# Kernel optimization log

Hardware: AMD Instinct MI355X
Metric: run time of the kernel (lower is better)

## Reference

```python
import jax, jax.numpy as jnp
import numpy as np

CHUNKS = 4  # number of input-feature chunks (seg_mode='input')
QMAX = 127.0  # symmetric int8 fake-quant range
EPS = 1e-8


def setup_inputs() -> dict:
    key = jax.random.key(0)
    k1, k2, k3 = jax.random.split(key, 3)
    B, S, F, O = 4, 4096, 4096, 4096
    x = jax.random.normal(k1, (B, S, F), dtype=jnp.float32)
    weight = jax.random.normal(k2, (O, F), dtype=jnp.float32) * 0.02
    bias = jax.random.normal(k3, (O,), dtype=jnp.float32) * 0.02
    return {"x": x, "weight": weight, "bias": bias}


def _fake_quant(t, scale):
    # symmetric int8 fake quantization: quantize then dequantize in float
    return jnp.clip(jnp.round(t / scale), -QMAX, QMAX) * scale


def reference(x, weight, bias):
    B, S, F = x.shape
    O = weight.shape[0]
    C = CHUNKS
    d = F // C

    # single weight quantizer (seg_mode='input'): per-tensor fake quant of full weight
    w_scale = jnp.maximum(jnp.max(jnp.abs(weight)) / QMAX, EPS)
    w_fq = _fake_quant(weight, w_scale)          # [O, F]
    wc = w_fq.reshape(O, C, d)                   # chunked along in_features

    # per-chunk input quantizers: one per input chunk
    xc = x.reshape(B, S, C, d)                   # split input along last dim
    x_scale = jnp.maximum(
        jnp.max(jnp.abs(xc), axis=(0, 1, 3), keepdims=True) / QMAX, EPS
    )                                            # [1,1,C,1] per-chunk scale
    x_fq = _fake_quant(xc, x_scale)              # [B, S, C, d]

    # chunked sub-matmuls summed over chunks (== sum_i x_i @ W_i^T), then bias
    out = jnp.einsum("bscd,ocd->bso", x_fq, wc) + bias
    return out
```

## Files before the change

kernel.cpp:

```cpp
#include <hip/hip_runtime.h>
#include <stdint.h>

static constexpr int M = 16384;
static constexpr int N = 4096;
static constexpr int K = 4096;
static constexpr int NCHUNK = 4;
static constexpr int CHUNK = 1024;

#define QMAXF 127.0f
#define EPSF 1e-8f

using i32x4 = __attribute__((ext_vector_type(4))) int;
using f32x4 = __attribute__((ext_vector_type(4))) float;

__device__ __forceinline__ void gld_lds16(const void* g, void* l) {
  __builtin_amdgcn_global_load_lds((const __attribute__((address_space(1))) void*)g,
                                   (__attribute__((address_space(3))) void*)l,
                                   16, 0, 0);
}

__device__ __forceinline__ float scale_from_bits(unsigned bits) {
  return fmaxf(__uint_as_float(bits) / QMAXF, EPSF);
}

__global__ void wabs_kernel(const float* __restrict__ w, unsigned* __restrict__ scales) {
  const int tid = blockIdx.x * blockDim.x + threadIdx.x;
  const int stride = gridDim.x * blockDim.x;
  const float4* w4 = (const float4*)w;
  const int n4 = (N * K) / 4;
  float m = 0.f;
  for (int i = tid; i < n4; i += stride) {
    float4 v = w4[i];
    m = fmaxf(m, fmaxf(fmaxf(fabsf(v.x), fabsf(v.y)), fmaxf(fabsf(v.z), fabsf(v.w))));
  }
  #pragma unroll
  for (int off = 32; off; off >>= 1) m = fmaxf(m, __shfl_down(m, off));
  __shared__ float sm[4];
  const int lane = threadIdx.x & 63, wv = threadIdx.x >> 6;
  if (lane == 0) sm[wv] = m;
  __syncthreads();
  if (threadIdx.x == 0) {
    m = fmaxf(fmaxf(sm[0], sm[1]), fmaxf(sm[2], sm[3]));
    atomicMax(scales + 0, __float_as_uint(m));
  }
}

__global__ void xabs_kernel(const float* __restrict__ x, unsigned* __restrict__ scales) {
  const int tid = blockIdx.x * blockDim.x + threadIdx.x;
  const int stride = gridDim.x * blockDim.x;
  const float4* x4 = (const float4*)x;
  const int n4 = (M * K) / 4;
  float m0 = 0.f, m1 = 0.f, m2 = 0.f, m3 = 0.f;
  for (int i = tid; i < n4; i += stride) {
    float4 v = x4[i];
    float a = fmaxf(fmaxf(fabsf(v.x), fabsf(v.y)), fmaxf(fabsf(v.z), fabsf(v.w)));
    const int c = (i >> 8) & 3;
    m0 = (c == 0) ? fmaxf(m0, a) : m0;
    m1 = (c == 1) ? fmaxf(m1, a) : m1;
    m2 = (c == 2) ? fmaxf(m2, a) : m2;
    m3 = (c == 3) ? fmaxf(m3, a) : m3;
  }
  #pragma unroll
  for (int off = 32; off; off >>= 1) {
    m0 = fmaxf(m0, __shfl_down(m0, off));
    m1 = fmaxf(m1, __shfl_down(m1, off));
    m2 = fmaxf(m2, __shfl_down(m2, off));
    m3 = fmaxf(m3, __shfl_down(m3, off));
  }
  __shared__ float sm[4][4];
  const int lane = threadIdx.x & 63, wv = threadIdx.x >> 6;
  if (lane == 0) { sm[wv][0] = m0; sm[wv][1] = m1; sm[wv][2] = m2; sm[wv][3] = m3; }
  __syncthreads();
  if (threadIdx.x < 4) {
    const int c = threadIdx.x;
    float v = fmaxf(fmaxf(sm[0][c], sm[1][c]), fmaxf(sm[2][c], sm[3][c]));
    atomicMax(scales + 1 + c, __float_as_uint(v));
  }
}

__device__ __forceinline__ unsigned quant_pack4(float4 v, float inv) {
  int q0 = (int)fminf(fmaxf(rintf(v.x * inv), -QMAXF), QMAXF);
  int q1 = (int)fminf(fmaxf(rintf(v.y * inv), -QMAXF), QMAXF);
  int q2 = (int)fminf(fmaxf(rintf(v.z * inv), -QMAXF), QMAXF);
  int q3 = (int)fminf(fmaxf(rintf(v.w * inv), -QMAXF), QMAXF);
  return (unsigned)(q0 & 0xff) | ((unsigned)(q1 & 0xff) << 8) |
         ((unsigned)(q2 & 0xff) << 16) | ((unsigned)(q3 & 0xff) << 24);
}

__global__ void quant_w_kernel(const float* __restrict__ w, const unsigned* __restrict__ scales,
                               char* __restrict__ wq) {
  const int tid = blockIdx.x * blockDim.x + threadIdx.x;
  const int stride = gridDim.x * blockDim.x;
  const int n4 = (N * K) / 4;
  const float inv = 1.0f / scale_from_bits(scales[0]);
  for (int i = tid; i < n4; i += stride) {
    float4 v = ((const float4*)w)[i];
    ((unsigned*)wq)[i] = quant_pack4(v, inv);
  }
}

__global__ void quant_x_kernel(const float* __restrict__ x, const unsigned* __restrict__ scales,
                               char* __restrict__ xq) {
  const int tid = blockIdx.x * blockDim.x + threadIdx.x;
  const int stride = gridDim.x * blockDim.x;
  const int n4 = (M * K) / 4;
  float inv[4];
  #pragma unroll
  for (int c = 0; c < 4; ++c) inv[c] = 1.0f / scale_from_bits(scales[1 + c]);
  for (int i = tid; i < n4; i += stride) {
    const int c = (i >> 8) & 3;
    float4 v = ((const float4*)x)[i];
    ((unsigned*)xq)[i] = quant_pack4(v, inv[c]);
  }
}

__global__ __launch_bounds__(256, 2)
void gemm_i8_kernel(const char* __restrict__ xq, const char* __restrict__ wq,
                    const float* __restrict__ bias, const unsigned* __restrict__ scales,
                    float* __restrict__ out) {
  __shared__ char As[128 * 64];
  __shared__ char Bs[128 * 64];

  const int tn = blockIdx.x;
  const int tm = blockIdx.y;
  const int t = threadIdx.x;
  const int lane = t & 63, wv = t >> 6;
  const int wr = wv >> 1, wc = wv & 1;
  const int l16 = lane & 15, quad = lane >> 4;

  const float wsc = scale_from_bits(scales[0]);
  float csc[NCHUNK];
  #pragma unroll
  for (int c = 0; c < NCHUNK; ++c) csc[c] = scale_from_bits(scales[1 + c]) * wsc;

  const char* aG = xq + (size_t)tm * 128 * K;
  const char* bG = wq + (size_t)tn * 128 * K;

  const int L0 = t, L1 = t + 256;
  char* aL0 = As + L0 * 16;  char* aL1 = As + L1 * 16;
  char* bL0 = Bs + L0 * 16;  char* bL1 = Bs + L1 * 16;
  const int kx0 = (L0 & 3) ^ ((L0 >> 3) & 3);
  const int kx1 = (L1 & 3) ^ ((L1 >> 3) & 3);
  const char* aG0 = aG + (L0 >> 2) * K + kx0 * 16;
  const char* aG1 = aG + (L1 >> 2) * K + kx1 * 16;
  const char* bG0 = bG + (L0 >> 2) * K + kx0 * 16;
  const char* bG1 = bG + (L1 >> 2) * K + kx1 * 16;

  const int rcol = (quad ^ ((l16 >> 1) & 3)) * 16;

  f32x4 facc[4][4];
  #pragma unroll
  for (int mi = 0; mi < 4; ++mi)
    #pragma unroll
    for (int ni = 0; ni < 4; ++ni) facc[mi][ni] = (f32x4)(0.f);

  for (int c = 0; c < NCHUNK; ++c) {
    i32x4 iacc[4][4];
    #pragma unroll
    for (int mi = 0; mi < 4; ++mi)
      #pragma unroll
      for (int ni = 0; ni < 4; ++ni) iacc[mi][ni] = (i32x4)(0);

    for (int kk = 0; kk < CHUNK / 64; ++kk) {
      const int ko = c * CHUNK + kk * 64;
      gld_lds16(aG0 + ko, aL0);
      gld_lds16(aG1 + ko, aL1);
      gld_lds16(bG0 + ko, bL0);
      gld_lds16(bG1 + ko, bL1);
      __syncthreads();

      i32x4 af[4], bf[4];
      #pragma unroll
      for (int mi = 0; mi < 4; ++mi)
        af[mi] = *(const i32x4*)(As + ((wr * 64 + mi * 16 + l16) * 64 + rcol));
      #pragma unroll
      for (int ni = 0; ni < 4; ++ni)
        bf[ni] = *(const i32x4*)(Bs + ((wc * 64 + ni * 16 + l16) * 64 + rcol));

      #pragma unroll
      for (int mi = 0; mi < 4; ++mi)
        #pragma unroll
        for (int ni = 0; ni < 4; ++ni)
          iacc[mi][ni] = __builtin_amdgcn_mfma_i32_16x16x64_i8(af[mi], bf[ni], iacc[mi][ni], 0, 0, 0);

      __syncthreads();
    }

    const float sc = csc[c];
    #pragma unroll
    for (int mi = 0; mi < 4; ++mi)
      #pragma unroll
      for (int ni = 0; ni < 4; ++ni)
        #pragma unroll
        for (int e = 0; e < 4; ++e)
          facc[mi][ni][e] += sc * (float)iacc[mi][ni][e];
  }

  #pragma unroll
  for (int ni = 0; ni < 4; ++ni) {
    const int col = tn * 128 + wc * 64 + ni * 16 + l16;
    const float bv = bias[col];
    #pragma unroll
    for (int mi = 0; mi < 4; ++mi) {
      const int row_base = tm * 128 + wr * 64 + mi * 16 + quad * 4;
      #pragma unroll
      for (int r = 0; r < 4; ++r)
        out[(size_t)(row_base + r) * N + col] = facc[mi][ni][r] + bv;
    }
  }
}

extern "C" void kernel_launch(void* const* d_in, const int* in_sizes, int n_in,
                              void* d_out, int out_size, void* d_ws, size_t ws_size,
                              hipStream_t stream) {
  const float* x = (const float*)d_in[0];
  const float* w = (const float*)d_in[1];
  const float* bias = (const float*)d_in[2];
  float* out = (float*)d_out;

  unsigned* scales = (unsigned*)d_ws;
  char* xq = (char*)d_ws + 64;
  char* wq = xq + (size_t)M * K;

  hipMemsetAsync(d_ws, 0, 64, stream);

  wabs_kernel<<<4096, 256, 0, stream>>>(w, scales);
  xabs_kernel<<<8192, 256, 0, stream>>>(x, scales);
  quant_w_kernel<<<4096, 256, 0, stream>>>(w, scales, wq);
  quant_x_kernel<<<16384, 256, 0, stream>>>(x, scales, xq);

  dim3 grid(N / 128, M / 128);
  gemm_i8_kernel<<<grid, 256, 0, stream>>>(xq, wq, bias, scales, out);
}
```

Measured before the change: 974.3 us.

## Merge prep kernels and triple-buffer a larger int8 GEMM tile with swizzled grid

Merges the four absmax and quantize kernels into two launches, each using a 5-way grid (four x chunks plus the weight). The int8 GEMM moves to 256x128x128 tiles with 512 threads, triple-buffered async global-to-LDS loads with explicit waitcnt, XOR-swizzled LDS, s_setprio around the MFMA blocks, and a block-index swizzle for L2 locality. This targets load latency and barrier stalls in the main matmul plus launch overhead in preprocessing, at the cost of more LDS and registers per block, which may limit occupancy.

```diff
diff --git a/kernel.cpp b/kernel.cpp
--- a/kernel.cpp
+++ b/kernel.cpp
@@ -7,6 +7,13 @@
 static constexpr int NCHUNK = 4;
 static constexpr int CHUNK = 1024;
 
+static constexpr int BM = 256, BN = 128, BK = 128;
+static constexpr int ABYTES = BM * BK;
+static constexpr int BBYTES = BN * BK;
+static constexpr int BUFB = ABYTES + BBYTES;
+static constexpr int NSTEP = K / BK;
+static constexpr int STEPS_PER_CHUNK = CHUNK / BK;
+
 #define QMAXF 127.0f
 #define EPSF 1e-8f
 
@@ -23,15 +30,35 @@
   return fmaxf(__uint_as_float(bits) / QMAXF, EPSF);
 }
 
-__global__ void wabs_kernel(const float* __restrict__ w, unsigned* __restrict__ scales) {
+__device__ __forceinline__ unsigned quant_pack4(float4 v, float inv) {
+  int q0 = (int)fminf(fmaxf(rintf(v.x * inv), -QMAXF), QMAXF);
+  int q1 = (int)fminf(fmaxf(rintf(v.y * inv), -QMAXF), QMAXF);
+  int q2 = (int)fminf(fmaxf(rintf(v.z * inv), -QMAXF), QMAXF);
+  int q3 = (int)fminf(fmaxf(rintf(v.w * inv), -QMAXF), QMAXF);
+  return (unsigned)(q0 & 0xff) | ((unsigned)(q1 & 0xff) << 8) |
+         ((unsigned)(q2 & 0xff) << 16) | ((unsigned)(q3 & 0xff) << 24);
+}
+
+__global__ void absmax_kernel(const float* __restrict__ x, const float* __restrict__ w,
+                              unsigned* __restrict__ scales) {
+  const int p = blockIdx.y;
   const int tid = blockIdx.x * blockDim.x + threadIdx.x;
   const int stride = gridDim.x * blockDim.x;
-  const float4* w4 = (const float4*)w;
-  const int n4 = (N * K) / 4;
+  const int total = (N * K) / 4;
   float m = 0.f;
-  for (int i = tid; i < n4; i += stride) {
-    float4 v = w4[i];
-    m = fmaxf(m, fmaxf(fmaxf(fabsf(v.x), fabsf(v.y)), fmaxf(fabsf(v.z), fabsf(v.w))));
+  if (p == 4) {
+    const float4* w4 = (const float4*)w;
+    for (int i = tid; i < total; i += stride) {
+      float4 v = w4[i];
+      m = fmaxf(m, fmaxf(fmaxf(fabsf(v.x), fabsf(v.y)), fmaxf(fabsf(v.z), fabsf(v.w))));
+    }
+  } else {
+    const float4* x4 = (const float4*)x;
+    for (int i = tid; i < total; i += stride) {
+      const int r = i >> 8, j = i & 255;
+      float4 v = x4[((size_t)r << 10) + (p << 8) + j];
+      m = fmaxf(m, fmaxf(fmaxf(fabsf(v.x), fabsf(v.y)), fmaxf(fabsf(v.z), fabsf(v.w))));
+    }
   }
   #pragma unroll
   for (int off = 32; off; off >>= 1) m = fmaxf(m, __shfl_down(m, off));
@@ -41,88 +68,44 @@
   __syncthreads();
   if (threadIdx.x == 0) {
     m = fmaxf(fmaxf(sm[0], sm[1]), fmaxf(sm[2], sm[3]));
-    atomicMax(scales + 0, __float_as_uint(m));
-  }
-}
-
-__global__ void xabs_kernel(const float* __restrict__ x, unsigned* __restrict__ scales) {
+    atomicMax(scales + (p == 4 ? 0 : 1 + p), __float_as_uint(m));
+  }
+}
+
+__global__ void quant_kernel(const float* __restrict__ x, const float* __restrict__ w,
+                             const unsigned* __restrict__ scales,
+                             char* __restrict__ xq, char* __restrict__ wq) {
+  const int p = blockIdx.y;
   const int tid = blockIdx.x * blockDim.x + threadIdx.x;
   const int stride = gridDim.x * blockDim.x;
-  const float4* x4 = (const float4*)x;
-  const int n4 = (M * K) / 4;
-  float m0 = 0.f, m1 = 0.f, m2 = 0.f, m3 = 0.f;
-  for (int i = tid; i < n4; i += stride) {
-    float4 v = x4[i];
-    float a = fmaxf(fmaxf(fabsf(v.x), fabsf(v.y)), fmaxf(fabsf(v.z), fabsf(v.w)));
-    const int c = (i >> 8) & 3;
-    m0 = (c == 0) ? fmaxf(m0, a) : m0;
-    m1 = (c == 1) ? fmaxf(m1, a) : m1;
-    m2 = (c == 2) ? fmaxf(m2, a) : m2;
-    m3 = (c == 3) ? fmaxf(m3, a) : m3;
-  }
-  #pragma unroll
-  for (int off = 32; off; off >>= 1) {
-    m0 = fmaxf(m0, __shfl_down(m0, off));
-    m1 = fmaxf(m1, __shfl_down(m1, off));
-    m2 = fmaxf(m2, __shfl_down(m2, off));
-    m3 = fmaxf(m3, __shfl_down(m3, off));
-  }
-  __shared__ float sm[4][4];
-  const int lane = threadIdx.x & 63, wv = threadIdx.x >> 6;
-  if (lane == 0) { sm[wv][0] = m0; sm[wv][1] = m1; sm[wv][2] = m2; sm[wv][3] = m3; }
-  __syncthreads();
-  if (threadIdx.x < 4) {
-    const int c = threadIdx.x;
-    float v = fmaxf(fmaxf(sm[0][c], sm[1][c]), fmaxf(sm[2][c], sm[3][c]));
-    atomicMax(scales + 1 + c, __float_as_uint(v));
-  }
-}
-
-__device__ __forceinline__ unsigned quant_pack4(float4 v, float inv) {
-  int q0 = (int)fminf(fmaxf(rintf(v.x * inv), -QMAXF), QMAXF);
-  int q1 = (int)fminf(fmaxf(rintf(v.y * inv), -QMAXF), QMAXF);
-  int q2 = (int)fminf(fmaxf(rintf(v.z * inv), -QMAXF), QMAXF);
-  int q3 = (int)fminf(fmaxf(rintf(v.w * inv), -QMAXF), QMAXF);
-  return (unsigned)(q0 & 0xff) | ((unsigned)(q1 & 0xff) << 8) |
-         ((unsigned)(q2 & 0xff) << 16) | ((unsigned)(q3 & 0xff) << 24);
-}
-
-__global__ void quant_w_kernel(const float* __restrict__ w, const unsigned* __restrict__ scales,
-                               char* __restrict__ wq) {
-  const int tid = blockIdx.x * blockDim.x + threadIdx.x;
-  const int stride = gridDim.x * blockDim.x;
-  const int n4 = (N * K) / 4;
-  const float inv = 1.0f / scale_from_bits(scales[0]);
-  for (int i = tid; i < n4; i += stride) {
-    float4 v = ((const float4*)w)[i];
-    ((unsigned*)wq)[i] = quant_pack4(v, inv);
-  }
-}
-
-__global__ void quant_x_kernel(const float* __restrict__ x, const unsigned* __restrict__ scales,
-                               char* __restrict__ xq) {
-  const int tid = blockIdx.x * blockDim.x + threadIdx.x;
-  const int stride = gridDim.x * blockDim.x;
-  const int n4 = (M * K) / 4;
-  float inv[4];
-  #pragma unroll
-  for (int c = 0; c < 4; ++c) inv[c] = 1.0f / scale_from_bits(scales[1 + c]);
-  for (int i = tid; i < n4; i += stride) {
-    const int c = (i >> 8) & 3;
-    float4 v = ((const float4*)x)[i];
-    ((unsigned*)xq)[i] = quant_pack4(v, inv[c]);
-  }
-}
-
-__global__ __launch_bounds__(256, 2)
+  const int total = (N * K) / 4;
+  const float inv = 1.0f / scale_from_bits(scales[p == 4 ? 0 : 1 + p]);
+  if (p == 4) {
+    const float4* w4 = (const float4*)w;
+    unsigned* wq4 = (unsigned*)wq;
+    for (int i = tid; i < total; i += stride) wq4[i] = quant_pack4(w4[i], inv);
+  } else {
+    const float4* x4 = (const float4*)x;
+    unsigned* xq4 = (unsigned*)xq;
+    for (int i = tid; i < total; i += stride) {
+      const int r = i >> 8, j = i & 255;
+      const size_t idx = ((size_t)r << 10) + (p << 8) + j;
+      xq4[idx] = quant_pack4(x4[idx], inv);
+    }
+  }
+}
+
+__global__ __launch_bounds__(512, 2)
 void gemm_i8_kernel(const char* __restrict__ xq, const char* __restrict__ wq,
                     const float* __restrict__ bias, const unsigned* __restrict__ scales,
                     float* __restrict__ out) {
-  __shared__ char As[128 * 64];
-  __shared__ char Bs[128 * 64];
-
-  const int tn = blockIdx.x;
-  const int tm = blockIdx.y;
+  __shared__ char lds[3 * BUFB];
+
+  const int bid = blockIdx.x;
+  const int swz = (bid & 7) * 256 + (bid >> 3);
+  const int tn = swz & 31;
+  const int tm = swz >> 5;
+
   const int t = threadIdx.x;
   const int lane = t & 63, wv = t >> 6;
   const int wr = wv >> 1, wc = wv & 1;
@@ -133,20 +116,41 @@
   #pragma unroll
   for (int c = 0; c < NCHUNK; ++c) csc[c] = scale_from_bits(scales[1 + c]) * wsc;
 
-  const char* aG = xq + (size_t)tm * 128 * K;
-  const char* bG = wq + (size_t)tn * 128 * K;
-
-  const int L0 = t, L1 = t + 256;
-  char* aL0 = As + L0 * 16;  char* aL1 = As + L1 * 16;
-  char* bL0 = Bs + L0 * 16;  char* bL1 = Bs + L1 * 16;
-  const int kx0 = (L0 & 3) ^ ((L0 >> 3) & 3);
-  const int kx1 = (L1 & 3) ^ ((L1 >> 3) & 3);
-  const char* aG0 = aG + (L0 >> 2) * K + kx0 * 16;
-  const char* aG1 = aG + (L1 >> 2) * K + kx1 * 16;
-  const char* bG0 = bG + (L0 >> 2) * K + kx0 * 16;
-  const char* bG1 = bG + (L1 >> 2) * K + kx1 * 16;
-
-  const int rcol = (quad ^ ((l16 >> 1) & 3)) * 16;
+  const char* aSrc[4]; unsigned aDst[4];
+  #pragma unroll
+  for (int j = 0; j < 4; ++j) {
+    const int L = t + j * 512;
+    const int row = L >> 3, colG = (L & 7) ^ (row & 7);
+    aSrc[j] = xq + (size_t)(tm * 256 + row) * K + colG * 16;
+    aDst[j] = (unsigned)(L * 16);
+  }
+  const char* bSrc[2]; unsigned bDst[2];
+  #pragma unroll
+  for (int j = 0; j < 2; ++j) {
+    const int L = t + j * 512;
+    const int row = L >> 3, colG = (L & 7) ^ (row & 7);
+    bSrc[j] = wq + (size_t)(tn * 128 + row) * K + colG * 16;
+    bDst[j] = (unsigned)(ABYTES + L * 16);
+  }
+
+  unsigned aoffs[2], boffs[2];
+  #pragma unroll
+  for (int kf = 0; kf < 2; ++kf) {
+    const unsigned cs = (unsigned)((((kf * 4 + quad) ^ (l16 & 7)) * 16));
+    aoffs[kf] = (unsigned)((wr * 64 + l16) * BK) + cs;
+    boffs[kf] = (unsigned)(ABYTES + (wc * 64 + l16) * BK) + cs;
+  }
+
+  auto issue = [&](unsigned bufOff) {
+    #pragma unroll
+    for (int j = 0; j < 4; ++j) gld_lds16(aSrc[j], lds + bufOff + aDst[j]);
+    #pragma unroll
+    for (int j = 0; j < 2; ++j) gld_lds16(bSrc[j], lds + bufOff + bDst[j]);
+    #pragma unroll
+    for (int j = 0; j < 4; ++j) aSrc[j] += BK;
+    #pragma unroll
+    for (int j = 0; j < 2; ++j) bSrc[j] += BK;
+  };
 
   f32x4 facc[4][4];
   #pragma unroll
@@ -154,6 +158,12 @@
     #pragma unroll
     for (int ni = 0; ni < 4; ++ni) facc[mi][ni] = (f32x4)(0.f);
 
+  issue(0);
+  issue(BUFB);
+  unsigned pfOff = 2 * BUFB;
+  unsigned rdOff = 0;
+
+  #pragma unroll
   for (int c = 0; c < NCHUNK; ++c) {
     i32x4 iacc[4][4];
     #pragma unroll
@@ -161,29 +171,41 @@
       #pragma unroll
       for (int ni = 0; ni < 4; ++ni) iacc[mi][ni] = (i32x4)(0);
 
-    for (int kk = 0; kk < CHUNK / 64; ++kk) {
-      const int ko = c * CHUNK + kk * 64;
-      gld_lds16(aG0 + ko, aL0);
-      gld_lds16(aG1 + ko, aL1);
-      gld_lds16(bG0 + ko, bL0);
-      gld_lds16(bG1 + ko, bL1);
-      __syncthreads();
-
-      i32x4 af[4], bf[4];
-      #pragma unroll
-      for (int mi = 0; mi < 4; ++mi)
-        af[mi] = *(const i32x4*)(As + ((wr * 64 + mi * 16 + l16) * 64 + rcol));
-      #pragma unroll
-      for (int ni = 0; ni < 4; ++ni)
-        bf[ni] = *(const i32x4*)(Bs + ((wc * 64 + ni * 16 + l16) * 64 + rcol));
-
-      #pragma unroll
-      for (int mi = 0; mi < 4; ++mi)
+    #pragma unroll 1
+    for (int kk = 0; kk < STEPS_PER_CHUNK; ++kk) {
+      const int tt = c * STEPS_PER_CHUNK + kk;
+      asm volatile("s_waitcnt lgkmcnt(0)" ::: "memory");
+      if (tt < NSTEP - 1) {
+        asm volatile("s_waitcnt vmcnt(6)" ::: "memory");
+      } else {
+        asm volatile("s_waitcnt vmcnt(0)" ::: "memory");
+      }
+      __builtin_amdgcn_s_barrier();
+      asm volatile("" ::: "memory");
+
+      if (tt <= NSTEP - 3) {
+        issue(pfOff);
+        pfOff = (pfOff == 2 * BUFB) ? 0u : pfOff + BUFB;
+      }
+
+      #pragma unroll
+      for (int kf = 0; kf < 2; ++kf) {
+        i32x4 af[4], bf[4];
+        #pragma unroll
+        for (int mi = 0; mi < 4; ++mi)
+          af[mi] = *(const i32x4*)(lds + rdOff + aoffs[kf] + mi * (16 * BK));
         #pragma unroll
         for (int ni = 0; ni < 4; ++ni)
-          iacc[mi][ni] = __builtin_amdgcn_mfma_i32_16x16x64_i8(af[mi], bf[ni], iacc[mi][ni], 0, 0, 0);
-
-      __syncthreads();
+          bf[ni] = *(const i32x4*)(lds + rdOff + boffs[kf] + ni * (16 * BK));
+        __builtin_amdgcn_s_setprio(1);
+        #pragma unroll
+        for (int mi = 0; mi < 4; ++mi)
+          #pragma unroll
+          for (int ni = 0; ni < 4; ++ni)
+            iacc[mi][ni] = __builtin_amdgcn_mfma_i32_16x16x64_i8(af[mi], bf[ni], iacc[mi][ni], 0, 0, 0);
+        __builtin_amdgcn_s_setprio(0);
+      }
+      rdOff = (rdOff == 2 * BUFB) ? 0u : rdOff + BUFB;
     }
 
     const float sc = csc[c];
@@ -202,10 +224,10 @@
     const float bv = bias[col];
     #pragma unroll
     for (int mi = 0; mi < 4; ++mi) {
-      const int row_base = tm * 128 + wr * 64 + mi * 16 + quad * 4;
-      #pragma unroll
-      for (int r = 0; r < 4; ++r)
-        out[(size_t)(row_base + r) * N + col] = facc[mi][ni][r] + bv;
+      const int row_base = tm * 256 + wr * 64 + mi * 16 + quad * 4;
+      #pragma unroll
+      for (int e = 0; e < 4; ++e)
+        out[(size_t)(row_base + e) * N + col] = facc[mi][ni][e] + bv;
     }
   }
 }
@@ -224,11 +246,9 @@
 
   hipMemsetAsync(d_ws, 0, 64, stream);
 
-  wabs_kernel<<<4096, 256, 0, stream>>>(w, scales);
-  xabs_kernel<<<8192, 256, 0, stream>>>(x, scales);
-  quant_w_kernel<<<4096, 256, 0, stream>>>(w, scales, wq);
-  quant_x_kernel<<<16384, 256, 0, stream>>>(x, scales, xq);
-
-  dim3 grid(N / 128, M / 128);
-  gemm_i8_kernel<<<grid, 256, 0, stream>>>(xq, wq, bias, scales, out);
-}
+  dim3 pgrid(2048, 5);
+  absmax_kernel<<<pgrid, 256, 0, stream>>>(x, w, scales);
+  quant_kernel<<<pgrid, 256, 0, stream>>>(x, w, scales, xq, wq);
+
+  gemm_i8_kernel<<<dim3(2048), 512, 0, stream>>>(xq, wq, bias, scales, out);
+}
```

Result: slower. 1.089 ms (+11.8%).
